# Kernel optimization log

Hardware: AMD Instinct MI355X
Metric: run time of the kernel (lower is better)

Reference implementation:

```python
import jax, jax.numpy as jnp
import numpy as np

B, H, N, D = 4, 16, 2048, 128  # batch, num_head, maxlen, head_dim (qkdim == vdim)
EPS = 1e-6


def _act(x):
    # '1+elu' kernel feature map
    return jax.nn.elu(x) + 1.0


def _simple_rms_norm(x):
    # SimpleRMSNorm over the last dim: x / sqrt(mean(x^2) + eps), no learned scale
    ms = jnp.mean(jnp.square(x), axis=-1, keepdims=True)
    return x * jax.lax.rsqrt(ms + EPS)


def setup_inputs() -> dict:
    key = jax.random.key(0)
    kq, kk, kv, km = jax.random.split(key, 4)
    Q = jax.random.normal(kq, (B, H, N, D), dtype=jnp.float32)
    K = jax.random.normal(kk, (B, H, N, D), dtype=jnp.float32)
    V = jax.random.normal(kv, (B, H, N, D), dtype=jnp.float32)
    mask = jax.random.uniform(km, (B, N), dtype=jnp.float32)
    return {"Q": Q, "K": K, "V": V, "mask": mask}


def reference(Q, K, V, mask):
    m = mask[:, None, :, None]           # (B, 1, N, 1)
    Qf = _act(Q)                          # (B, H, N, D)
    Kf = _act(K) * m                      # masked feature-mapped keys
    Vf = V * m                            # masked values
    # non-causal linear attention: KV = sum_n K_n (x) V_n ; out = Q @ KV
    KV = jnp.einsum('bhnd,bhne->bhde', Kf, Vf)    # (B, H, D, D)
    out = jnp.einsum('bhde,bhnd->bhne', KV, Qf)   # (B, H, N, D)
    return _simple_rms_norm(out)
```

## Files before the change

### kernel.cpp

```cpp
#include <hip/hip_runtime.h>
#include <hip/hip_bf16.h>

#define NB 4
#define NH 16
#define NBH 64
#define NSEQ 2048
#define DD 128
#define EPS 1e-6f

typedef __bf16 bf16x8 __attribute__((ext_vector_type(8)));
typedef __bf16 bf16x4 __attribute__((ext_vector_type(4)));
typedef float  f32x4  __attribute__((ext_vector_type(4)));

__device__ __forceinline__ float elu1(float x) {
    return x > 0.f ? x + 1.f : __expf(x);
}

__global__ __launch_bounds__(512) void kv_partial_kernel(
    const float* __restrict__ K, const float* __restrict__ V,
    const float* __restrict__ mask, float* __restrict__ part)
{
    __shared__ __bf16 KfT[128 * 72];
    __shared__ __bf16 VfT[128 * 72];
    __shared__ float  mloc[256];

    const int s  = blockIdx.x;
    const int bh = blockIdx.y;
    const int b  = bh >> 4;
    const int t  = threadIdx.x;
    const int n0 = s * 256;

    if (t < 256) mloc[t] = mask[b * NSEQ + n0 + t];

    const int d    = t & 127;
    const int qtr  = t >> 7;
    const int lane = t & 63;
    const int w    = t >> 6;
    const int quad = lane >> 4;
    const int col  = lane & 15;

    f32x4 acc[8];
    #pragma unroll
    for (int nt = 0; nt < 8; ++nt) acc[nt] = (f32x4){0.f, 0.f, 0.f, 0.f};

    const float* Kb = K + ((size_t)bh * NSEQ + n0) * DD;
    const float* Vb = V + ((size_t)bh * NSEQ + n0) * DD;

    for (int sub = 0; sub < 4; ++sub) {
        __syncthreads();
        #pragma unroll
        for (int r0 = 0; r0 < 16; r0 += 4) {
            bf16x4 kp, vp;
            #pragma unroll
            for (int j = 0; j < 4; ++j) {
                int nl = sub * 64 + qtr * 16 + r0 + j;
                float m  = mloc[nl];
                float kx = Kb[(size_t)nl * DD + d];
                float vx = Vb[(size_t)nl * DD + d];
                kp[j] = (__bf16)(elu1(kx) * m);
                vp[j] = (__bf16)(vx * m);
            }
            int nn = qtr * 16 + r0;
            *(bf16x4*)&KfT[d * 72 + nn] = kp;
            *(bf16x4*)&VfT[d * 72 + nn] = vp;
        }
        __syncthreads();

        #pragma unroll
        for (int kk = 0; kk < 2; ++kk) {
            int k0 = kk * 32 + quad * 8;
            bf16x8 a = *(bf16x8*)&VfT[(w * 16 + col) * 72 + k0];
            #pragma unroll
            for (int nt = 0; nt < 8; ++nt) {
                bf16x8 bb = *(bf16x8*)&KfT[(nt * 16 + col) * 72 + k0];
                acc[nt] = __builtin_amdgcn_mfma_f32_16x16x32_bf16(a, bb, acc[nt], 0, 0, 0);
            }
        }
    }

    float* po = part + (((size_t)bh * 8 + s) << 14);
    #pragma unroll
    for (int r = 0; r < 4; ++r) {
        int e = w * 16 + quad * 4 + r;
        #pragma unroll
        for (int nt = 0; nt < 8; ++nt)
            po[e * 128 + nt * 16 + col] = acc[nt][r];
    }
}

__global__ __launch_bounds__(256) void kv_reduce_kernel(
    const float* __restrict__ part, __bf16* __restrict__ kvt)
{
    int gid = blockIdx.x * 256 + threadIdx.x;
    int i   = gid * 4;
    int bh  = i >> 14;
    int ii  = i & 16383;
    const float* p = part + (((size_t)bh * 8) << 14) + ii;
    f32x4 sum = (f32x4){0.f, 0.f, 0.f, 0.f};
    #pragma unroll
    for (int s = 0; s < 8; ++s)
        sum += *(const f32x4*)(p + ((size_t)s << 14));
    bf16x4 o;
    o[0] = (__bf16)sum[0]; o[1] = (__bf16)sum[1];
    o[2] = (__bf16)sum[2]; o[3] = (__bf16)sum[3];
    *(bf16x4*)&kvt[i] = o;
}

__global__ __launch_bounds__(256) void qkv_norm_kernel(
    const float* __restrict__ Q, const __bf16* __restrict__ kvt,
    float* __restrict__ out)
{
    __shared__ __bf16 KVT[128 * 136];
    __shared__ __bf16 Qf[64 * 136];

    const int bh   = blockIdx.y;
    const int row0 = blockIdx.x * 64;
    const int t    = threadIdx.x;
    const int lane = t & 63;
    const int w    = t >> 6;
    const int quad = lane >> 4;
    const int col  = lane & 15;

    {
        const __bf16* src = kvt + ((size_t)bh << 14);
        #pragma unroll
        for (int i = 0; i < 8; ++i) {
            int idx = i * 256 + t;
            int e   = idx >> 4;
            int dd  = (idx & 15) * 8;
            *(bf16x8*)&KVT[e * 136 + dd] = *(const bf16x8*)&src[e * 128 + dd];
        }
    }
    {
        const float* Qb = Q + ((size_t)bh * NSEQ + row0) * DD;
        #pragma unroll
        for (int i = 0; i < 8; ++i) {
            int idx = i * 256 + t;
            int r   = idx >> 5;
            int dd  = (idx & 31) * 4;
            f32x4 q = *(const f32x4*)&Qb[r * DD + dd];
            bf16x4 qq;
            qq[0] = (__bf16)elu1(q[0]); qq[1] = (__bf16)elu1(q[1]);
            qq[2] = (__bf16)elu1(q[2]); qq[3] = (__bf16)elu1(q[3]);
            *(bf16x4*)&Qf[r * 136 + dd] = qq;
        }
    }
    __syncthreads();

    f32x4 acc[8];
    #pragma unroll
    for (int et = 0; et < 8; ++et) acc[et] = (f32x4){0.f, 0.f, 0.f, 0.f};

    #pragma unroll
    for (int kk = 0; kk < 4; ++kk) {
        int k0 = kk * 32 + quad * 8;
        bf16x8 a = *(bf16x8*)&Qf[(w * 16 + col) * 136 + k0];
        #pragma unroll
        for (int et = 0; et < 8; ++et) {
            bf16x8 bb = *(bf16x8*)&KVT[(et * 16 + col) * 136 + k0];
            acc[et] = __builtin_amdgcn_mfma_f32_16x16x32_bf16(a, bb, acc[et], 0, 0, 0);
        }
    }

    float* ob = out + ((size_t)bh * NSEQ + row0) * DD;
    #pragma unroll
    for (int r = 0; r < 4; ++r) {
        float p = 0.f;
        #pragma unroll
        for (int et = 0; et < 8; ++et) p += acc[et][r] * acc[et][r];
        p += __shfl_xor(p, 1);
        p += __shfl_xor(p, 2);
        p += __shfl_xor(p, 4);
        p += __shfl_xor(p, 8);
        float scale = rsqrtf(p * (1.0f / 128.0f) + EPS);
        int row = w * 16 + quad * 4 + r;
        #pragma unroll
        for (int et = 0; et < 8; ++et)
            ob[row * DD + et * 16 + col] = acc[et][r] * scale;
    }
}

extern "C" void kernel_launch(void* const* d_in, const int* in_sizes, int n_in,
                              void* d_out, int out_size, void* d_ws, size_t ws_size,
                              hipStream_t stream) {
    const float* Q    = (const float*)d_in[0];
    const float* K    = (const float*)d_in[1];
    const float* V    = (const float*)d_in[2];
    const float* mask = (const float*)d_in[3];
    float* out = (float*)d_out;

    float*  part = (float*)d_ws;
    __bf16* kvt  = (__bf16*)((char*)d_ws + (size_t)NBH * 8 * 16384 * 4);

    kv_partial_kernel<<<dim3(8, NBH), 512, 0, stream>>>(K, V, mask, part);
    kv_reduce_kernel<<<1024, 256, 0, stream>>>(part, kvt);
    qkv_norm_kernel<<<dim3(32, NBH), 256, 0, stream>>>(Q, kvt, out);
}
```

Measured before the change: 240.0 us.

## Vectorize K/V loads with swizzled LDS staging and register-prefetch; load Q fragments directly

The KV partial kernel now reads K and V as float4 vectors into registers. It stages 128-row chunks into XOR-swizzled LDS tiles and prefetches the second chunk while the first chunk's MFMAs run, which replaces four scalar-load sub-iterations and the mask staging in shared memory. The Q·KV kernel drops its Q shared-memory tile: each lane loads its own MFMA A-operand fragment from global memory straight into registers and applies elu there. Occupancy hints are added to both kernels. The risks are higher register pressure and a larger LDS footprint per block.

```diff
diff --git a/kernel.cpp b/kernel.cpp
--- a/kernel.cpp
+++ b/kernel.cpp
@@ -1,8 +1,6 @@
 #include <hip/hip_runtime.h>
 #include <hip/hip_bf16.h>
 
-#define NB 4
-#define NH 16
 #define NBH 64
 #define NSEQ 2048
 #define DD 128
@@ -16,67 +14,102 @@
     return x > 0.f ? x + 1.f : __expf(x);
 }
 
-__global__ __launch_bounds__(512) void kv_partial_kernel(
+__device__ __forceinline__ int swz(int r) {
+    return ((r >> 2) & 7) ^ ((r & 1) << 2);
+}
+
+__global__ __launch_bounds__(512, 4) void kv_partial_kernel(
     const float* __restrict__ K, const float* __restrict__ V,
     const float* __restrict__ mask, float* __restrict__ part)
 {
-    __shared__ __bf16 KfT[128 * 72];
-    __shared__ __bf16 VfT[128 * 72];
-    __shared__ float  mloc[256];
-
-    const int s  = blockIdx.x;
-    const int bh = blockIdx.y;
-    const int b  = bh >> 4;
-    const int t  = threadIdx.x;
-    const int n0 = s * 256;
-
-    if (t < 256) mloc[t] = mask[b * NSEQ + n0 + t];
-
-    const int d    = t & 127;
-    const int qtr  = t >> 7;
+    __shared__ __bf16 KfT[128 * 128];
+    __shared__ __bf16 VfT[128 * 128];
+
+    const int s    = blockIdx.x;
+    const int bh   = blockIdx.y;
+    const int b    = bh >> 4;
+    const int t    = threadIdx.x;
+    const int c    = t & 31;
+    const int rg   = t >> 5;
     const int lane = t & 63;
     const int w    = t >> 6;
     const int quad = lane >> 4;
     const int col  = lane & 15;
+    const int n0   = s * 256;
+
+    const f32x4* K4   = (const f32x4*)(K + ((size_t)bh * NSEQ + n0) * DD);
+    const f32x4* V4   = (const f32x4*)(V + ((size_t)bh * NSEQ + n0) * DD);
+    const float* mrow = mask + b * NSEQ + n0;
 
     f32x4 acc[8];
     #pragma unroll
     for (int nt = 0; nt < 8; ++nt) acc[nt] = (f32x4){0.f, 0.f, 0.f, 0.f};
 
-    const float* Kb = K + ((size_t)bh * NSEQ + n0) * DD;
-    const float* Vb = V + ((size_t)bh * NSEQ + n0) * DD;
-
-    for (int sub = 0; sub < 4; ++sub) {
-        __syncthreads();
-        #pragma unroll
-        for (int r0 = 0; r0 < 16; r0 += 4) {
-            bf16x4 kp, vp;
+    const int arow = w * 16 + col;
+    const int aidx = (arow * 128) | (swz(arow) << 3);
+    int bidx[8];
+    #pragma unroll
+    for (int nt = 0; nt < 8; ++nt) {
+        int r = nt * 16 + col;
+        bidx[nt] = (r * 128) | (swz(r) << 3);
+    }
+
+    f32x4 kr[8], vr[8];
+    float mv[8];
+
+    auto stage = [&]() {
+        #pragma unroll
+        for (int i = 0; i < 4; ++i) {
+            bf16x8 kc, vc;
             #pragma unroll
-            for (int j = 0; j < 4; ++j) {
-                int nl = sub * 64 + qtr * 16 + r0 + j;
-                float m  = mloc[nl];
-                float kx = Kb[(size_t)nl * DD + d];
-                float vx = Vb[(size_t)nl * DD + d];
-                kp[j] = (__bf16)(elu1(kx) * m);
-                vp[j] = (__bf16)(vx * m);
+            for (int j = 0; j < 8; ++j) {
+                float m = mv[j];
+                kc[j] = (__bf16)(elu1(kr[j][i]) * m);
+                vc[j] = (__bf16)(vr[j][i] * m);
             }
-            int nn = qtr * 16 + r0;
-            *(bf16x4*)&KfT[d * 72 + nn] = kp;
-            *(bf16x4*)&VfT[d * 72 + nn] = vp;
-        }
-        __syncthreads();
-
-        #pragma unroll
-        for (int kk = 0; kk < 2; ++kk) {
+            int d  = 4 * c + i;
+            int wi = d * 128 + 8 * (rg ^ swz(d));
+            *(bf16x8*)&KfT[wi] = kc;
+            *(bf16x8*)&VfT[wi] = vc;
+        }
+    };
+
+    auto mfma_tile = [&]() {
+        #pragma unroll
+        for (int kk = 0; kk < 4; ++kk) {
             int k0 = kk * 32 + quad * 8;
-            bf16x8 a = *(bf16x8*)&VfT[(w * 16 + col) * 72 + k0];
+            bf16x8 a = *(bf16x8*)&VfT[aidx ^ k0];
             #pragma unroll
             for (int nt = 0; nt < 8; ++nt) {
-                bf16x8 bb = *(bf16x8*)&KfT[(nt * 16 + col) * 72 + k0];
+                bf16x8 bb = *(bf16x8*)&KfT[bidx[nt] ^ k0];
                 acc[nt] = __builtin_amdgcn_mfma_f32_16x16x32_bf16(a, bb, acc[nt], 0, 0, 0);
             }
         }
-    }
+    };
+
+    #pragma unroll
+    for (int j = 0; j < 8; ++j) {
+        int row = rg * 8 + j;
+        kr[j] = K4[row * 32 + c];
+        vr[j] = V4[row * 32 + c];
+        mv[j] = mrow[row];
+    }
+    stage();
+    __syncthreads();
+
+    #pragma unroll
+    for (int j = 0; j < 8; ++j) {
+        int row = 128 + rg * 8 + j;
+        kr[j] = K4[row * 32 + c];
+        vr[j] = V4[row * 32 + c];
+        mv[j] = mrow[row];
+    }
+
+    mfma_tile();
+    __syncthreads();
+    stage();
+    __syncthreads();
+    mfma_tile();
 
     float* po = part + (((size_t)bh * 8 + s) << 14);
     #pragma unroll
@@ -106,12 +139,11 @@
     *(bf16x4*)&kvt[i] = o;
 }
 
-__global__ __launch_bounds__(256) void qkv_norm_kernel(
+__global__ __launch_bounds__(256, 4) void qkv_norm_kernel(
     const float* __restrict__ Q, const __bf16* __restrict__ kvt,
     float* __restrict__ out)
 {
     __shared__ __bf16 KVT[128 * 136];
-    __shared__ __bf16 Qf[64 * 136];
 
     const int bh   = blockIdx.y;
     const int row0 = blockIdx.x * 64;
@@ -121,6 +153,15 @@
     const int quad = lane >> 4;
     const int col  = lane & 15;
 
+    const int row = row0 + w * 16 + col;
+    const f32x4* q4 = (const f32x4*)(Q + ((size_t)bh * NSEQ + row) * DD);
+    f32x4 qr[8];
+    #pragma unroll
+    for (int kk = 0; kk < 4; ++kk) {
+        qr[2 * kk]     = q4[kk * 8 + quad * 2];
+        qr[2 * kk + 1] = q4[kk * 8 + quad * 2 + 1];
+    }
+
     {
         const __bf16* src = kvt + ((size_t)bh << 14);
         #pragma unroll
@@ -131,21 +172,19 @@
             *(bf16x8*)&KVT[e * 136 + dd] = *(const bf16x8*)&src[e * 128 + dd];
         }
     }
-    {
-        const float* Qb = Q + ((size_t)bh * NSEQ + row0) * DD;
-        #pragma unroll
-        for (int i = 0; i < 8; ++i) {
-            int idx = i * 256 + t;
-            int r   = idx >> 5;
-            int dd  = (idx & 31) * 4;
-            f32x4 q = *(const f32x4*)&Qb[r * DD + dd];
-            bf16x4 qq;
-            qq[0] = (__bf16)elu1(q[0]); qq[1] = (__bf16)elu1(q[1]);
-            qq[2] = (__bf16)elu1(q[2]); qq[3] = (__bf16)elu1(q[3]);
-            *(bf16x4*)&Qf[r * 136 + dd] = qq;
-        }
-    }
-    __syncthreads();
+    __syncthreads();
+
+    bf16x8 a[4];
+    #pragma unroll
+    for (int kk = 0; kk < 4; ++kk) {
+        #pragma unroll
+        for (int h = 0; h < 2; ++h) {
+            f32x4 q = qr[2 * kk + h];
+            #pragma unroll
+            for (int u = 0; u < 4; ++u)
+                a[kk][h * 4 + u] = (__bf16)elu1(q[u]);
+        }
+    }
 
     f32x4 acc[8];
     #pragma unroll
@@ -154,11 +193,10 @@
     #pragma unroll
     for (int kk = 0; kk < 4; ++kk) {
         int k0 = kk * 32 + quad * 8;
-        bf16x8 a = *(bf16x8*)&Qf[(w * 16 + col) * 136 + k0];
         #pragma unroll
         for (int et = 0; et < 8; ++et) {
             bf16x8 bb = *(bf16x8*)&KVT[(et * 16 + col) * 136 + k0];
-            acc[et] = __builtin_amdgcn_mfma_f32_16x16x32_bf16(a, bb, acc[et], 0, 0, 0);
+            acc[et] = __builtin_amdgcn_mfma_f32_16x16x32_bf16(a[kk], bb, acc[et], 0, 0, 0);
         }
     }
 
@@ -173,10 +211,10 @@
         p += __shfl_xor(p, 4);
         p += __shfl_xor(p, 8);
         float scale = rsqrtf(p * (1.0f / 128.0f) + EPS);
-        int row = w * 16 + quad * 4 + r;
+        int orow = w * 16 + quad * 4 + r;
         #pragma unroll
         for (int et = 0; et < 8; ++et)
-            ob[row * DD + et * 16 + col] = acc[et][r] * scale;
+            ob[orow * DD + et * 16 + col] = acc[et][r] * scale;
     }
 }
 
```

After: 251.1 us. 4.6% more time.
